# Kernel tuning notes

Hardware: AMD Instinct MI355X
Metric: run time of the kernel (lower is better)

## Reference

```python
import jax, jax.numpy as jnp
import numpy as np
import math

NLAT, NLON = 46, 90      # equiangular grid (in_shape == out_shape)
CH = 256                 # channels == kdim == vdim
BATCH = 1

def _cc_weights(n):
    # Clenshaw-Curtis quadrature weights (Waldvogel), nodes cos(k*pi/(n-1)); matches torch-harmonics equiangular grid
    n1 = n - 1
    N = np.arange(1, n1, 2)
    l = len(N)
    m = n1 - l
    v = np.concatenate([2.0 / N / (N - 2), [1.0 / N[-1]], np.zeros(m)])
    v = -v[:-1] - v[-1:0:-1]
    g0 = -np.ones(n1)
    g0[l] += n1
    g0[m] += n1
    g = g0 / (n1 ** 2 - 1 + (n1 % 2))
    w = np.fft.ifft(v + g).real
    return np.concatenate([w, w[:1]])

def _precompute_sparsity():
    # replicates _precompute_neighborhood_sparsity_s2: YZY-rotated north pole indicator within theta_cutoff
    lats = np.linspace(0.0, math.pi, NLAT)               # colatitudes of equiangular grid
    quad = (2.0 * math.pi / NLON) * _cc_weights(NLAT)    # per-latitude quadrature weights
    cutoff = math.pi / (NLAT - 1)                        # default theta_cutoff
    lons = np.linspace(0.0, 2.0 * math.pi, NLON + 1)[:-1]
    rows, cols = [], []
    for t in range(NLAT):
        a = -lats[t]
        beta = lons[None, :]
        gamma = lats[:, None]
        z = -np.cos(beta) * np.sin(a) * np.sin(gamma) + np.cos(a) * np.cos(gamma)
        x = np.cos(a) * np.cos(beta) * np.sin(gamma) + np.cos(gamma) * np.sin(a)
        y = np.sin(beta) * np.sin(gamma)
        nrm = np.sqrt(x * x + y * y + z * z)
        theta = np.arccos(np.clip(z / nrm, -1.0, 1.0))
        ii, jj = np.nonzero(theta <= cutoff)
        rows.append(np.full(ii.shape, t, dtype=np.int64))
        cols.append(ii * NLON + jj)
    row_ids = np.concatenate(rows).astype(np.int32)   # CSR row id per nnz (sorted)
    col_idx = np.concatenate(cols).astype(np.int32)   # flattened input index (at wo=0)
    return row_ids, col_idx, quad.astype(np.float32)

def setup_inputs() -> dict:
    key = jax.random.key(0)
    ks = jax.random.split(key, 9)
    row_ids, col_idx, quad = _precompute_sparsity()
    scale = 0.02  # sane init scale (module uses raw randn; trained weights would be O(this))
    return {
        "qo": jax.random.normal(ks[0], (BATCH, CH, NLAT, NLON), dtype=jnp.float32),
        "ki": jax.random.normal(ks[1], (BATCH, CH, NLAT, NLON), dtype=jnp.float32),
        "vi": jax.random.normal(ks[2], (BATCH, CH, NLAT, NLON), dtype=jnp.float32),
        "q_w": jax.random.normal(ks[3], (CH, CH), dtype=jnp.float32) * scale,
        "k_w": jax.random.normal(ks[4], (CH, CH), dtype=jnp.float32) * scale,
        "v_w": jax.random.normal(ks[5], (CH, CH), dtype=jnp.float32) * scale,
        "q_b": jax.random.normal(ks[6], (CH,), dtype=jnp.float32) * scale,
        "k_b": jax.random.normal(ks[7], (CH,), dtype=jnp.float32) * scale,
        "v_b": jax.random.normal(ks[8], (CH,), dtype=jnp.float32) * scale,
        "quad_w": jnp.asarray(quad),
        "row_ids": jnp.asarray(row_ids),
        "col_idx": jnp.asarray(col_idx),
    }

def reference(qo, ki, vi, q_w, k_w, v_w, q_b, k_b, v_b, quad_w, row_ids, col_idx):
    nlat, nlon = qo.shape[2], qo.shape[3]
    # 1x1 conv projections (F.conv2d with [out,in,1,1] kernels)
    q = jnp.einsum("kc,bchw->bkhw", q_w, qo) + q_b[None, :, None, None]
    k = jnp.einsum("kc,bchw->bkhw", k_w, ki) + k_b[None, :, None, None]
    v = jnp.einsum("vc,bchw->bvhw", v_w, vi) + v_b[None, :, None, None]

    hi = col_idx // nlon                                   # [N] input latitude per nnz
    wi0 = col_idx % nlon                                   # [N] input longitude at wo=0
    wo = jnp.arange(nlon)
    wi = (wi0[:, None] + wo[None, :]) % nlon               # [N, nlon] longitudes rotated by output lon

    kg = k[:, :, hi[:, None], wi]                          # [B, kdim, N, nlon] gathered keys
    qg = q[:, :, row_ids, :]                               # [B, kdim, N, nlon] query of owning output row
    qdotk = jnp.einsum("bcnw,bcnw->nbw", qg, kg)           # [N, B, nlon]

    # quadrature-weighted softmax over each output point's neighborhood (segment = output latitude row)
    seg_max = jax.ops.segment_max(qdotk, row_ids, num_segments=nlat, indices_are_sorted=True)
    seg_max = jax.lax.stop_gradient(seg_max)               # max shift cancels exactly in the ratio
    alpha = jnp.exp(qdotk - seg_max[row_ids]) * quad_w[hi][:, None, None]   # [N, B, nlon]
    denom = jax.ops.segment_sum(alpha, row_ids, num_segments=nlat, indices_are_sorted=True)  # [nlat, B, nlon]

    vg = jnp.transpose(v[:, :, hi[:, None], wi], (2, 0, 1, 3))   # [N, B, vdim, nlon]
    num = jax.ops.segment_sum(alpha[:, :, None, :] * vg, row_ids, num_segments=nlat, indices_are_sorted=True)
    out = num / denom[:, :, None, :]                       # [nlat, B, vdim, nlon]
    return jnp.transpose(out, (1, 2, 0, 3))                # [B, vdim, nlat, nlon]
```

## Files before the change

### kernel.cpp

```cpp
#include <hip/hip_runtime.h>
#include <math.h>

#define NLAT 46
#define NLON 90
#define CH   256
#define HW   (NLAT*NLON)
#define HWP  4160
#define HWT  32
#define NHT  130
#define XSTR 264

#define LIGHT_PER_XCD 473
#define SLOTS_PER_XCD (45 + LIGHT_PER_XCD)

typedef __attribute__((ext_vector_type(8))) short short8;
typedef __attribute__((ext_vector_type(4))) float floatx4;

__device__ __forceinline__ ushort f2bf(float f){
  uint u = __float_as_uint(f);
  u += 0x7fff + ((u >> 16) & 1);
  return (ushort)(u >> 16);
}
__device__ __forceinline__ float bf2f(ushort u){
  return __uint_as_float(((uint)u) << 16);
}
__device__ __forceinline__ float bf2fs(short s){
  return __uint_as_float(((uint)(ushort)s) << 16);
}

__device__ __forceinline__ int lower_bound_i(const int* __restrict__ a, int n, int key){
  int lo = 0, hi = n;
  while (lo < hi){ int mid = (lo + hi) >> 1; if (a[mid] < key) lo = mid + 1; else hi = mid; }
  return lo;
}

__global__ __launch_bounds__(256) void fproj_kernel(
    const float* __restrict__ qo, const float* __restrict__ ki, const float* __restrict__ vi,
    const float* __restrict__ qw, const float* __restrict__ kw, const float* __restrict__ vw,
    const float* __restrict__ qb, const float* __restrict__ kb, const float* __restrict__ vb,
    ushort* __restrict__ qP, ushort* __restrict__ kP, ushort* __restrict__ vP)
{
  const float* X; const float* Wf; const float* Bias; ushort* Out;
  if (blockIdx.y == 0){ X = qo; Wf = qw; Bias = qb; Out = qP; }
  else if (blockIdx.y == 1){ X = ki; Wf = kw; Bias = kb; Out = kP; }
  else { X = vi; Wf = vw; Bias = vb; Out = vP; }

  __shared__ ushort Xs[HWT][XSTR];

  const int tid = threadIdx.x;
  const int hw0 = blockIdx.x * HWT;

  {
    int hwL = tid & 31;
    int cb  = tid >> 5;
    int hw  = hw0 + hwL;
    bool ok = hw < HW;
    const float* Xp = X + (size_t)(cb*32)*HW + (ok ? hw : 0);
    #pragma unroll
    for (int g = 0; g < 4; g++){
      short8 pk;
      #pragma unroll
      for (int u = 0; u < 8; u++){
        float f = ok ? Xp[(size_t)(g*8 + u)*HW] : 0.f;
        pk[u] = (short)f2bf(f);
      }
      *(short8*)(&Xs[hwL][cb*32 + g*8]) = pk;
    }
  }
  __syncthreads();

  const int lane = tid & 63;
  const int wave = tid >> 6;
  const int lm = lane & 15;
  const int lq = lane >> 4;
  const int kout_w = wave * 64;

  const float* Apf = Wf + (size_t)(kout_w + lm)*CH + lq*8;

  floatx4 acc[4][2];
  #pragma unroll
  for (int i = 0; i < 4; i++)
    #pragma unroll
    for (int j = 0; j < 2; j++) acc[i][j] = (floatx4){0,0,0,0};

  #pragma unroll
  for (int k0 = 0; k0 < 8; k0++){
    short8 a[4], b[2];
    #pragma unroll
    for (int i = 0; i < 4; i++){
      const float* p = Apf + (size_t)i*16*CH + k0*32;
      float4 w0 = *(const float4*)p;
      float4 w1 = *(const float4*)(p + 4);
      a[i][0] = (short)f2bf(w0.x); a[i][1] = (short)f2bf(w0.y);
      a[i][2] = (short)f2bf(w0.z); a[i][3] = (short)f2bf(w0.w);
      a[i][4] = (short)f2bf(w1.x); a[i][5] = (short)f2bf(w1.y);
      a[i][6] = (short)f2bf(w1.z); a[i][7] = (short)f2bf(w1.w);
    }
    #pragma unroll
    for (int j = 0; j < 2; j++)
      b[j] = *(const short8*)(&Xs[j*16 + lm][lq*8 + k0*32]);
    #pragma unroll
    for (int i = 0; i < 4; i++)
      #pragma unroll
      for (int j = 0; j < 2; j++)
        acc[i][j] = __builtin_amdgcn_mfma_f32_16x16x32_bf16(a[i], b[j], acc[i][j], 0, 0, 0);
  }

  #pragma unroll
  for (int i = 0; i < 4; i++){
    int kout = kout_w + i*16 + lq*4;
    float4 bias = *(const float4*)(Bias + kout);
    #pragma unroll
    for (int j = 0; j < 2; j++){
      int hw = hw0 + j*16 + lm;
      if (hw < HW){
        ushort4 o;
        o.x = f2bf(acc[i][j][0] + bias.x);
        o.y = f2bf(acc[i][j][1] + bias.y);
        o.z = f2bf(acc[i][j][2] + bias.z);
        o.w = f2bf(acc[i][j][3] + bias.w);
        *(ushort4*)(Out + (size_t)hw*CH + kout) = o;
      }
    }
  }
}

__global__ __launch_bounds__(256) void attn_kernel(
    const ushort* __restrict__ qP, const ushort* __restrict__ kP, const ushort* __restrict__ vP,
    const float* __restrict__ quad_w, const int* __restrict__ row_ids,
    const int* __restrict__ col_idx, int nnz, float* __restrict__ out)
{
  const int bid  = blockIdx.x;
  const int xcd  = bid & 7;
  const int slot = bid >> 3;

  int t, wo;
  if (slot < 45){
    int hu   = xcd * 45 + slot;
    int hidx = hu / 90;
    t  = (hidx < 2) ? hidx : 42 + hidx;
    wo = hu - hidx * 90;
  } else {
    int lu = xcd * LIGHT_PER_XCD + (slot - 45);
    if (lu >= 42 * NLON) return;
    int li = lu / NLON;
    t  = li + 2;
    wo = lu - li * NLON;
  }

  const int tid  = threadIdx.x;
  const int lane = tid & 63;
  const int wave = tid >> 6;
  const int g    = lane >> 4;
  const int gl   = lane & 15;

  const int start = lower_bound_i(row_ids, nnz, t);
  const int end   = lower_bound_i(row_ids, nnz, t + 1);

  float qf[16];
  {
    const ushort* qrow = qP + (size_t)(t * NLON + wo) * CH + gl*16;
    short8 q0 = *(const short8*)(qrow);
    short8 q1 = *(const short8*)(qrow + 8);
    #pragma unroll
    for (int u = 0; u < 8; u++){ qf[u] = bf2fs(q0[u]); qf[8+u] = bf2fs(q1[u]); }
  }

  float den = 0.f;
  float acc[16];
  #pragma unroll
  for (int u = 0; u < 16; u++) acc[u] = 0.f;

  for (int n0 = start + wave*4 + g; n0 < end; n0 += 16){
    int ci = col_idx[n0];
    int hi = ci / NLON;
    int wi = ci - hi*NLON + wo; if (wi >= NLON) wi -= NLON;
    size_t off = ((size_t)hi*NLON + wi) * CH + gl*16;

    const short8* kp8 = (const short8*)(kP + off);
    short8 k0 = kp8[0], k1 = kp8[1];
    float s = 0.f;
    #pragma unroll
    for (int u = 0; u < 8; u++){
      s += qf[u]   * bf2fs(k0[u]);
      s += qf[8+u] * bf2fs(k1[u]);
    }
    s += __shfl_xor(s, 1, 64);
    s += __shfl_xor(s, 2, 64);
    s += __shfl_xor(s, 4, 64);
    s += __shfl_xor(s, 8, 64);

    float e = __expf(s) * quad_w[hi];
    const short8* vp8 = (const short8*)(vP + off);
    short8 v0 = vp8[0], v1 = vp8[1];
    den += e;
    #pragma unroll
    for (int u = 0; u < 8; u++){
      acc[u]   += e * bf2fs(v0[u]);
      acc[8+u] += e * bf2fs(v1[u]);
    }
  }

  #pragma unroll
  for (int u = 0; u < 16; u++){
    acc[u] += __shfl_xor(acc[u], 16, 64);
    acc[u] += __shfl_xor(acc[u], 32, 64);
  }
  den += __shfl_xor(den, 16, 64);
  den += __shfl_xor(den, 32, 64);

  __shared__ float sden[4];
  __shared__ float sacc[4][CH];
  if (lane == 0) sden[wave] = den;
  if (g == 0){
    #pragma unroll
    for (int u = 0; u < 16; u++) sacc[wave][gl*16 + u] = acc[u];
  }
  __syncthreads();

  const float D   = sden[0] + sden[1] + sden[2] + sden[3];
  const float num = sacc[0][tid] + sacc[1][tid] + sacc[2][tid] + sacc[3][tid];
  out[(size_t)tid * HW + t * NLON + wo] = num / D;
}

extern "C" void kernel_launch(void* const* d_in, const int* in_sizes, int n_in,
                              void* d_out, int out_size, void* d_ws, size_t ws_size,
                              hipStream_t stream)
{
  const float* qo   = (const float*)d_in[0];
  const float* ki   = (const float*)d_in[1];
  const float* vi   = (const float*)d_in[2];
  const float* qw   = (const float*)d_in[3];
  const float* kw   = (const float*)d_in[4];
  const float* vw   = (const float*)d_in[5];
  const float* qb   = (const float*)d_in[6];
  const float* kb   = (const float*)d_in[7];
  const float* vb   = (const float*)d_in[8];
  const float* quad = (const float*)d_in[9];
  const int* row_ids = (const int*)d_in[10];
  const int* col_idx = (const int*)d_in[11];
  const int nnz = in_sizes[10];

  ushort* ws = (ushort*)d_ws;
  const size_t TSZ = (size_t)HWP * CH;
  ushort* qP = ws;  ushort* kP = qP + TSZ;  ushort* vP = kP + TSZ;

  fproj_kernel<<<dim3(NHT, 3), 256, 0, stream>>>(qo, ki, vi, qw, kw, vw, qb, kb, vb, qP, kP, vP);
  attn_kernel<<<dim3(8 * SLOTS_PER_XCD), 256, 0, stream>>>(qP, kP, vP, quad, row_ids, col_idx, nnz, (float*)d_out);
}
```

Measured before the change: 123.3 us.

## Pack four output longitudes per light attention block and stage neighbor indices in LDS

In the attention kernel, light rows now assign one wave per output longitude, so each block handles four outputs instead of one block per output, and the cross-wave LDS reduction is removed for those rows. Neighbor indices and quadrature weights are decoded once into shared memory, which replaces per-visit integer division and global loads. The projection kernel tile grows from 32 to 64 spatial positions per block, so each block reuses its weight fragments over more MFMAs. The risks are lower parallelism per output on light rows, which gives longer serial loops per wave, and more register use in the projection kernel.

```diff
diff --git a/kernel.cpp b/kernel.cpp
--- a/kernel.cpp
+++ b/kernel.cpp
@@ -6,12 +6,15 @@
 #define CH   256
 #define HW   (NLAT*NLON)
 #define HWP  4160
-#define HWT  32
-#define NHT  130
+#define HWT  64
+#define NHT  65
 #define XSTR 264
 
-#define LIGHT_PER_XCD 473
-#define SLOTS_PER_XCD (45 + LIGHT_PER_XCD)
+#define HEAVY_PER_XCD 45
+#define LIGHT_GROUPS_PER_ROW 23
+#define LIGHT_UNITS   (42*LIGHT_GROUPS_PER_ROW)
+#define LIGHT_PER_XCD 121
+#define SLOTS_PER_XCD (HEAVY_PER_XCD + LIGHT_PER_XCD)
 
 typedef __attribute__((ext_vector_type(8))) short short8;
 typedef __attribute__((ext_vector_type(4))) float floatx4;
@@ -20,9 +23,6 @@
   uint u = __float_as_uint(f);
   u += 0x7fff + ((u >> 16) & 1);
   return (ushort)(u >> 16);
-}
-__device__ __forceinline__ float bf2f(ushort u){
-  return __uint_as_float(((uint)u) << 16);
 }
 __device__ __forceinline__ float bf2fs(short s){
   return __uint_as_float(((uint)(ushort)s) << 16);
@@ -51,20 +51,20 @@
   const int hw0 = blockIdx.x * HWT;
 
   {
-    int hwL = tid & 31;
-    int cb  = tid >> 5;
+    int hwL = tid & 63;
+    int cb  = tid >> 6;
     int hw  = hw0 + hwL;
     bool ok = hw < HW;
-    const float* Xp = X + (size_t)(cb*32)*HW + (ok ? hw : 0);
-    #pragma unroll
-    for (int g = 0; g < 4; g++){
+    const float* Xp = X + (size_t)(cb*64)*HW + (ok ? hw : 0);
+    #pragma unroll
+    for (int gq = 0; gq < 8; gq++){
       short8 pk;
       #pragma unroll
       for (int u = 0; u < 8; u++){
-        float f = ok ? Xp[(size_t)(g*8 + u)*HW] : 0.f;
+        float f = ok ? Xp[(size_t)(gq*8 + u)*HW] : 0.f;
         pk[u] = (short)f2bf(f);
       }
-      *(short8*)(&Xs[hwL][cb*32 + g*8]) = pk;
+      *(short8*)(&Xs[hwL][cb*64 + gq*8]) = pk;
     }
   }
   __syncthreads();
@@ -77,15 +77,15 @@
 
   const float* Apf = Wf + (size_t)(kout_w + lm)*CH + lq*8;
 
-  floatx4 acc[4][2];
+  floatx4 acc[4][4];
   #pragma unroll
   for (int i = 0; i < 4; i++)
     #pragma unroll
-    for (int j = 0; j < 2; j++) acc[i][j] = (floatx4){0,0,0,0};
+    for (int j = 0; j < 4; j++) acc[i][j] = (floatx4){0,0,0,0};
 
   #pragma unroll
   for (int k0 = 0; k0 < 8; k0++){
-    short8 a[4], b[2];
+    short8 a[4], b[4];
     #pragma unroll
     for (int i = 0; i < 4; i++){
       const float* p = Apf + (size_t)i*16*CH + k0*32;
@@ -97,12 +97,12 @@
       a[i][6] = (short)f2bf(w1.z); a[i][7] = (short)f2bf(w1.w);
     }
     #pragma unroll
-    for (int j = 0; j < 2; j++)
+    for (int j = 0; j < 4; j++)
       b[j] = *(const short8*)(&Xs[j*16 + lm][lq*8 + k0*32]);
     #pragma unroll
     for (int i = 0; i < 4; i++)
       #pragma unroll
-      for (int j = 0; j < 2; j++)
+      for (int j = 0; j < 4; j++)
         acc[i][j] = __builtin_amdgcn_mfma_f32_16x16x32_bf16(a[i], b[j], acc[i][j], 0, 0, 0);
   }
 
@@ -111,7 +111,7 @@
     int kout = kout_w + i*16 + lq*4;
     float4 bias = *(const float4*)(Bias + kout);
     #pragma unroll
-    for (int j = 0; j < 2; j++){
+    for (int j = 0; j < 4; j++){
       int hw = hw0 + j*16 + lm;
       if (hw < HW){
         ushort4 o;
@@ -125,6 +125,47 @@
   }
 }
 
+__device__ __forceinline__ void load_q16(const ushort* __restrict__ qP, int row, int gl, float* qf){
+  const ushort* qrow = qP + (size_t)row * CH + gl*16;
+  short8 q0 = *(const short8*)(qrow);
+  short8 q1 = *(const short8*)(qrow + 8);
+  #pragma unroll
+  for (int u = 0; u < 8; u++){ qf[u] = bf2fs(q0[u]); qf[8+u] = bf2fs(q1[u]); }
+}
+
+__device__ __forceinline__ void visit(
+    const ushort* __restrict__ kP, const ushort* __restrict__ vP,
+    const uint* s_p, const float* s_qw,
+    int n, int wo, int gl, const float* qf, float& den, float* acc)
+{
+  uint p  = s_p[n];
+  int base = (int)(p & 0xffffu);
+  int wi0  = (int)(p >> 16);
+  int adj  = base + wo - ((wi0 + wo >= NLON) ? NLON : 0);
+  size_t off = (size_t)adj * CH + gl*16;
+  const short8* kp8 = (const short8*)(kP + off);
+  short8 k0 = kp8[0], k1 = kp8[1];
+  float s = 0.f;
+  #pragma unroll
+  for (int u = 0; u < 8; u++){
+    s += qf[u]   * bf2fs(k0[u]);
+    s += qf[8+u] * bf2fs(k1[u]);
+  }
+  s += __shfl_xor(s, 1, 64);
+  s += __shfl_xor(s, 2, 64);
+  s += __shfl_xor(s, 4, 64);
+  s += __shfl_xor(s, 8, 64);
+  float e = __expf(s) * s_qw[n];
+  const short8* vp8 = (const short8*)(vP + off);
+  short8 v0 = vp8[0], v1 = vp8[1];
+  den += e;
+  #pragma unroll
+  for (int u = 0; u < 8; u++){
+    acc[u]   += e * bf2fs(v0[u]);
+    acc[8+u] += e * bf2fs(v1[u]);
+  }
+}
+
 __global__ __launch_bounds__(256) void attn_kernel(
     const ushort* __restrict__ qP, const ushort* __restrict__ kP, const ushort* __restrict__ vP,
     const float* __restrict__ quad_w, const int* __restrict__ row_ids,
@@ -134,18 +175,20 @@
   const int xcd  = bid & 7;
   const int slot = bid >> 3;
 
-  int t, wo;
-  if (slot < 45){
-    int hu   = xcd * 45 + slot;
-    int hidx = hu / 90;
-    t  = (hidx < 2) ? hidx : 42 + hidx;
-    wo = hu - hidx * 90;
+  int t, wo0, heavy;
+  if (slot < HEAVY_PER_XCD){
+    heavy = 1;
+    int hu   = xcd * HEAVY_PER_XCD + slot;
+    int hidx = hu / NLON;
+    t   = (hidx < 2) ? hidx : 42 + hidx;
+    wo0 = hu - hidx * NLON;
   } else {
-    int lu = xcd * LIGHT_PER_XCD + (slot - 45);
-    if (lu >= 42 * NLON) return;
-    int li = lu / NLON;
-    t  = li + 2;
-    wo = lu - li * NLON;
+    heavy = 0;
+    int lu = xcd * LIGHT_PER_XCD + (slot - HEAVY_PER_XCD);
+    if (lu >= LIGHT_UNITS) return;
+    int li = lu / LIGHT_GROUPS_PER_ROW;
+    t   = li + 2;
+    wo0 = (lu - li * LIGHT_GROUPS_PER_ROW) * 4;
   }
 
   const int tid  = threadIdx.x;
@@ -156,71 +199,83 @@
 
   const int start = lower_bound_i(row_ids, nnz, t);
   const int end   = lower_bound_i(row_ids, nnz, t + 1);
-
-  float qf[16];
-  {
-    const ushort* qrow = qP + (size_t)(t * NLON + wo) * CH + gl*16;
-    short8 q0 = *(const short8*)(qrow);
-    short8 q1 = *(const short8*)(qrow + 8);
-    #pragma unroll
-    for (int u = 0; u < 8; u++){ qf[u] = bf2fs(q0[u]); qf[8+u] = bf2fs(q1[u]); }
-  }
-
-  float den = 0.f;
-  float acc[16];
-  #pragma unroll
-  for (int u = 0; u < 16; u++) acc[u] = 0.f;
-
-  for (int n0 = start + wave*4 + g; n0 < end; n0 += 16){
-    int ci = col_idx[n0];
-    int hi = ci / NLON;
-    int wi = ci - hi*NLON + wo; if (wi >= NLON) wi -= NLON;
-    size_t off = ((size_t)hi*NLON + wi) * CH + gl*16;
-
-    const short8* kp8 = (const short8*)(kP + off);
-    short8 k0 = kp8[0], k1 = kp8[1];
-    float s = 0.f;
-    #pragma unroll
-    for (int u = 0; u < 8; u++){
-      s += qf[u]   * bf2fs(k0[u]);
-      s += qf[8+u] * bf2fs(k1[u]);
-    }
-    s += __shfl_xor(s, 1, 64);
-    s += __shfl_xor(s, 2, 64);
-    s += __shfl_xor(s, 4, 64);
-    s += __shfl_xor(s, 8, 64);
-
-    float e = __expf(s) * quad_w[hi];
-    const short8* vp8 = (const short8*)(vP + off);
-    short8 v0 = vp8[0], v1 = vp8[1];
-    den += e;
-    #pragma unroll
-    for (int u = 0; u < 8; u++){
-      acc[u]   += e * bf2fs(v0[u]);
-      acc[8+u] += e * bf2fs(v1[u]);
-    }
-  }
-
-  #pragma unroll
-  for (int u = 0; u < 16; u++){
-    acc[u] += __shfl_xor(acc[u], 16, 64);
-    acc[u] += __shfl_xor(acc[u], 32, 64);
-  }
-  den += __shfl_xor(den, 16, 64);
-  den += __shfl_xor(den, 32, 64);
-
+  const int nv    = end - start;
+
+  __shared__ uint  s_p[256];
+  __shared__ float s_qw[256];
   __shared__ float sden[4];
   __shared__ float sacc[4][CH];
-  if (lane == 0) sden[wave] = den;
-  if (g == 0){
-    #pragma unroll
-    for (int u = 0; u < 16; u++) sacc[wave][gl*16 + u] = acc[u];
+
+  for (int n = tid; n < nv; n += 256){
+    int ci  = col_idx[start + n];
+    int hi  = ci / NLON;
+    int wi0 = ci - hi * NLON;
+    s_p[n]  = ((uint)wi0 << 16) | (uint)(hi * NLON + wi0);
+    s_qw[n] = quad_w[hi];
   }
   __syncthreads();
 
-  const float D   = sden[0] + sden[1] + sden[2] + sden[3];
-  const float num = sacc[0][tid] + sacc[1][tid] + sacc[2][tid] + sacc[3][tid];
-  out[(size_t)tid * HW + t * NLON + wo] = num / D;
+  if (heavy){
+    float qf[16];
+    load_q16(qP, t * NLON + wo0, gl, qf);
+    float den = 0.f;
+    float acc[16];
+    #pragma unroll
+    for (int u = 0; u < 16; u++) acc[u] = 0.f;
+
+    for (int n = wave*4 + g; n < nv; n += 16)
+      visit(kP, vP, s_p, s_qw, n, wo0, gl, qf, den, acc);
+
+    #pragma unroll
+    for (int u = 0; u < 16; u++){
+      acc[u] += __shfl_xor(acc[u], 16, 64);
+      acc[u] += __shfl_xor(acc[u], 32, 64);
+    }
+    den += __shfl_xor(den, 16, 64);
+    den += __shfl_xor(den, 32, 64);
+
+    if (lane == 0) sden[wave] = den;
+    if (g == 0){
+      #pragma unroll
+      for (int u = 0; u < 16; u++) sacc[wave][gl*16 + u] = acc[u];
+    }
+    __syncthreads();
+
+    const float D   = sden[0] + sden[1] + sden[2] + sden[3];
+    const float num = sacc[0][tid] + sacc[1][tid] + sacc[2][tid] + sacc[3][tid];
+    out[(size_t)tid * HW + t * NLON + wo0] = num / D;
+  } else {
+    const int wo = wo0 + wave;
+    if (wo >= NLON) return;
+
+    float qf[16];
+    load_q16(qP, t * NLON + wo, gl, qf);
+    float den = 0.f;
+    float acc[16];
+    #pragma unroll
+    for (int u = 0; u < 16; u++) acc[u] = 0.f;
+
+    for (int n = g; n < nv; n += 4)
+      visit(kP, vP, s_p, s_qw, n, wo, gl, qf, den, acc);
+
+    #pragma unroll
+    for (int u = 0; u < 16; u++){
+      acc[u] += __shfl_xor(acc[u], 16, 64);
+      acc[u] += __shfl_xor(acc[u], 32, 64);
+    }
+    den += __shfl_xor(den, 16, 64);
+    den += __shfl_xor(den, 32, 64);
+
+    const float invD = 1.0f / den;
+    #pragma unroll
+    for (int j = 0; j < 4; j++){
+      float v01 = (g & 1) ? acc[4 + j]  : acc[j];
+      float v23 = (g & 1) ? acc[12 + j] : acc[8 + j];
+      float val = (g & 2) ? v23 : v01;
+      int c = (gl << 4) + (g << 2) + j;
+      out[(size_t)c * HW + t * NLON + wo] = val * invD;
+    }
+  }
 }
 
 extern "C" void kernel_launch(void* const* d_in, const int* in_sizes, int n_in,
```

New measurement: 121.5 us. No clear change (-1.5%).
